# Performance work log

Measured on AMD Instinct MI355X. Metric: run time of the kernel, lower is better.

Reference implementation:

```python
import jax, jax.numpy as jnp
import numpy as np

N = 20000    # nodes
F = 64       # channels (num_features)
Z = 10       # species
DEG = 16
E = N * DEG  # edges
RD = 8       # radial_dim
EPS = 0.25   # epsilon (avg-degree normalization)
SQRT3 = 3.0 ** 0.5


def setup_inputs() -> dict:
    key = jax.random.key(0)
    ks = jax.random.split(key, 22)
    g = lambda i, shape, s=1.0: jax.random.normal(ks[i], shape, jnp.float32) * s
    return dict(
        vectors=g(0, (E, 3)),
        node_s=g(1, (N, F)),
        node_v=g(2, (N, F, 3)),
        radial_embed=jax.random.uniform(ks[3], (E, RD), jnp.float32),
        senders=jax.random.randint(ks[4], (E,), 0, N),
        receivers=jax.random.randint(ks[5], (E,), 0, N),
        species_counts=jnp.full((Z,), N // Z, dtype=jnp.int32),
        Wup0=g(6, (F, F)), Wup1=g(7, (F, F)),
        R1=g(8, (RD, 64)), R2=g(9, (64, 64)), R3=g(10, (64, 64)), R4=g(11, (64, 4 * F)),
        Wd0=g(12, (F, F)), Wd1=g(13, (F, F)),
        Ws0=g(14, (Z, F, F)), Ws1=g(15, (Z, F, F)),
        Wsc=g(16, (Z, 9, F)), Proj=g(17, (9, 9), 1.0 / 3.0),
        Wl0=g(18, (F, F)), Wl1=g(19, (F, F)),
        Wr=g(20, (F, 1)),
    )


def _forward(vectors, node_s, node_v, radial_embed, senders, receivers,
             species_counts, Wup0, Wup1, R1, R2, R3, R4, Wd0, Wd1,
             Ws0, Ws1, Wsc, Proj, Wl0, Wl1, Wr):
    inv = 1.0 / np.sqrt(F)
    # species index per node (counts -> contiguous blocks), like jnp.repeat in SymmetricContraction
    sidx = jnp.repeat(jnp.arange(Z), species_counts, total_repeat_length=N)

    # spherical harmonics l=0 (constant 1, folded into weights) and l=1
    r = jnp.linalg.norm(vectors, axis=-1, keepdims=True)
    Y1 = SQRT3 * vectors / r                              # (E,3)

    # species-indexed skip connection on input feats
    skip_s = jnp.einsum('nf,nfg->ng', node_s, Ws0[sidx]) * inv
    skip_v = jnp.einsum('nfi,nfg->ngi', node_v, Ws1[sidx]) * inv

    # linear_up (per-irrep channel mixing)
    hs = (node_s @ Wup0) * inv                            # (N,F)
    hv = jnp.einsum('nfi,fg->ngi', node_v, Wup1) * inv    # (N,F,3)

    # radial MLP -> per-edge, per-path, per-channel TP weights (weight_numel = 4*F)
    a = jax.nn.silu(radial_embed @ R1)
    a = jax.nn.silu(a @ R2)
    a = jax.nn.silu(a @ R3)
    w = (a @ R4).reshape(E, 4, F)

    # channelwise tensor product: gather senders, 4 CG paths, scatter to receivers
    es = hs[senders]                                      # (E,F)
    ev = hv[senders]                                      # (E,F,3)
    m_s = w[:, 0] * es + w[:, 1] * (jnp.einsum('efi,ei->ef', ev, Y1) / SQRT3)
    m_v = w[:, 2][..., None] * ev + w[:, 3][..., None] * (es[..., None] * Y1[:, None, :]) / SQRT3
    hs = jax.ops.segment_sum(m_s, receivers, num_segments=N) * EPS
    hv = jax.ops.segment_sum(m_v, receivers, num_segments=N) * EPS

    # linear_down
    hs = (hs @ Wd0) * inv
    hv = jnp.einsum('nfi,fg->ngi', hv, Wd1) * inv

    # symmetric contraction (correlation 1..3), species-keyed weights through fixed projection
    wsc = jnp.einsum('zpu,pb->zbu', Wsc, Proj)[sidx]      # (N,9,F)
    vv = jnp.sum(hv * hv, -1)                             # (N,F)
    bs = jnp.stack([hs, hs * hs, vv, hs ** 3, hs * vv], axis=1)                    # (N,5,F)
    bv = jnp.stack([hv, hs[..., None] * hv, (hs * hs)[..., None] * hv,
                    vv[..., None] * hv], axis=1)                                   # (N,4,F,3)
    cs = jnp.einsum('nbf,nbf->nf', bs, wsc[:, :5])
    cv = jnp.einsum('nbfi,nbf->nfi', bv, wsc[:, 5:])

    # linear_sc
    cs = (cs @ Wl0) * inv
    cv = jnp.einsum('nfi,fg->ngi', cv, Wl1) * inv

    # add skip
    h_s = cs + skip_s
    h_v = cv + skip_v

    # readout (0e -> 1x0e; only scalars participate)
    out = (h_s @ Wr) * inv                                # (N,1)
    return out, h_s, h_v


def reference(vectors, node_s, node_v, radial_embed, senders, receivers,
              species_counts, Wup0, Wup1, R1, R2, R3, R4, Wd0, Wd1,
              Ws0, Ws1, Wsc, Proj, Wl0, Wl1, Wr):
    return _forward(vectors, node_s, node_v, radial_embed, senders, receivers,
                    species_counts, Wup0, Wup1, R1, R2, R3, R4, Wd0, Wd1,
                    Ws0, Ws1, Wsc, Proj, Wl0, Wl1, Wr)
```

## Files before the change

### kernel.cpp

```cpp
#include <hip/hip_runtime.h>
#include <hip/hip_bf16.h>
#include <math.h>

#define N_NODES 20000
#define FCH 64
#define ZSP 10
#define E_EDGES 320000
#define CHUNK 160000
#define RDIM 8
#define EPSC 0.25f
#define SQRT3C 1.7320508075688772f
#define INV_SQRT3C 0.57735026918962576f
#define INV_F 0.125f

#define OFF_HSUP   0
#define OFF_HVUP   (N_NODES*64)
#define OFF_SKS    (OFF_HVUP + N_NODES*192)
#define OFF_SKV    (OFF_SKS + N_NODES*64)
#define OFF_HSMID  (OFF_SKV + N_NODES*192)
#define OFF_HVMID  (OFF_HSMID + N_NODES*64)
#define OFF_WSCP   (OFF_HVMID + N_NODES*192)
#define OFF_FRAGS  (OFF_WSCP + ZSP*576)
#define OFF_WBUF   (OFF_FRAGS + 13312)
#define OFF_CSR    (OFF_WBUF + CHUNK*128)
#define OFF_WF     (OFF_CSR + 2*CHUNK*4 + 400260)
#define CSR_CNT0   0
#define CSR_CNT1   20000
#define CSR_PTR0   40000
#define CSR_PTR1   60001
#define CSR_SEID   80002
#define CSR_AUX    400002

#define SU_WSC   5760
#define SU_PREP  (SU_WSC + 3328)
#define SU_PREP2 (SU_PREP + 26624)
#define SU_HIST  (SU_PREP2 + E_EDGES)

typedef __attribute__((ext_vector_type(8))) short bhalf8;
typedef __attribute__((ext_vector_type(4))) float f32x4;

__device__ __forceinline__ float silu_f(float x) {
    float e = __builtin_amdgcn_exp2f(x * -1.442695040888963f);
    return x * __builtin_amdgcn_rcpf(1.0f + e);
}

__device__ __forceinline__ unsigned short f2bf(float x) {
    unsigned int u = __float_as_uint(x);
    unsigned int r = u + 0x7FFFu + ((u >> 16) & 1u);
    return (unsigned short)(r >> 16);
}

__device__ __forceinline__ unsigned int pack_bf2(float lo, float hi) {
    __hip_bfloat162 b = __float22bfloat162_rn(make_float2(lo, hi));
    return *(unsigned int*)&b;
}

__device__ __forceinline__ void split_f32(float x, short& h, short& l) {
    unsigned int u = __float_as_uint(x);
    unsigned int hb = u & 0xFFFF0000u;
    h = (short)(u >> 16);
    float r = x - __uint_as_float(hb);
    l = (short)(__float_as_uint(r) >> 16);
}

__device__ __forceinline__ int species_of(int n, const int* counts) {
    int acc = 0, s = ZSP - 1;
#pragma unroll
    for (int z = 0; z < ZSP; z++) {
        int c = counts[z];
        if (n >= acc && n < acc + c) s = z;
        acc += c;
    }
    return s;
}

__global__ __launch_bounds__(256) void k_setup(
    const float* __restrict__ Wsc, const float* __restrict__ Proj, float* __restrict__ wscp,
    const float* __restrict__ R1, const float* __restrict__ R2,
    const float* __restrict__ R3, const float* __restrict__ R4,
    unsigned short* __restrict__ frags,
    const float* __restrict__ Wup0, const float* __restrict__ Wup1,
    const float* __restrict__ Ws0, const float* __restrict__ Ws1,
    const float* __restrict__ Wd0, const float* __restrict__ Wd1,
    const float* __restrict__ Wl0, const float* __restrict__ Wl1,
    unsigned short* __restrict__ wf,
    const int* __restrict__ receivers, int* __restrict__ csr) {
    int gid = blockIdx.x * 256 + threadIdx.x;
    if (gid < SU_WSC) {
        int z = gid / 576, t = gid % 576;
        int b = t >> 6, u = t & 63;
        float acc = 0.f;
#pragma unroll
        for (int p = 0; p < 9; p++) acc += Wsc[z * 576 + p * 64 + u] * Proj[p * 9 + b];
        wscp[z * 576 + b * 64 + u] = acc;
    } else if (gid < SU_PREP) {
        int id = gid - SU_WSC;
        int lane = id & 63, fi = id >> 6;
        int quad = lane >> 4, l15 = lane & 15;
        const float* W;
        int s, t, N;
        bool r1 = false;
        if (fi < 4)       { W = R1; s = 0; t = fi; N = 64; r1 = true; }
        else if (fi < 12) { W = R2; int x = fi - 4;  s = x >> 2; t = x & 3;  N = 64; }
        else if (fi < 20) { W = R3; int x = fi - 12; s = x >> 2; t = x & 3;  N = 64; }
        else              { W = R4; int x = fi - 20; s = x >> 4; t = x & 15; N = 256; }
        unsigned int v[4];
#pragma unroll
        for (int jj = 0; jj < 4; jj++) {
            unsigned short pk2[2];
#pragma unroll
            for (int o = 0; o < 2; o++) {
                int j = jj * 2 + o;
                int k = s * 32 + quad * 8 + j, n = t * 16 + l15;
                float val = (r1 && k >= RDIM) ? 0.f : W[k * N + n];
                pk2[o] = f2bf(val);
            }
            v[jj] = (unsigned int)pk2[0] | ((unsigned int)pk2[1] << 16);
        }
        uint4 pk; pk.x = v[0]; pk.y = v[1]; pk.z = v[2]; pk.w = v[3];
        ((uint4*)frags)[id] = pk;
    } else if (gid < SU_PREP2) {
        int id = gid - SU_PREP;
        int lane = id & 63, slot = id >> 6;
        int t = slot & 3, s = (slot >> 2) & 1, part = (slot >> 3) & 1, mat = slot >> 4;
        int quad = lane >> 4, l15 = lane & 15;
        const float* W;
        if (mat == 0)       W = Wup0;
        else if (mat == 1)  W = Wup1;
        else if (mat < 12)  W = Ws0 + (mat - 2) * 4096;
        else if (mat < 22)  W = Ws1 + (mat - 12) * 4096;
        else if (mat == 22) W = Wd0;
        else if (mat == 23) W = Wd1;
        else if (mat == 24) W = Wl0;
        else                W = Wl1;
        unsigned int v[4];
#pragma unroll
        for (int jj = 0; jj < 4; jj++) {
            unsigned short pk2[2];
#pragma unroll
            for (int o = 0; o < 2; o++) {
                int j = jj * 2 + o;
                int k = s * 32 + quad * 8 + j, n = t * 16 + l15;
                float x = W[k * 64 + n];
                short h, l;
                split_f32(x, h, l);
                pk2[o] = part == 0 ? (unsigned short)h : (unsigned short)l;
            }
            v[jj] = (unsigned int)pk2[0] | ((unsigned int)pk2[1] << 16);
        }
        uint4 pk; pk.x = v[0]; pk.y = v[1]; pk.z = v[2]; pk.w = v[3];
        ((uint4*)wf)[id] = pk;
    } else if (gid < SU_HIST) {
        int e = gid - SU_PREP2;
        int base = (e < CHUNK) ? CSR_CNT0 : CSR_CNT1;
        atomicAdd(&csr[base + receivers[e]], 1);
    }
}

__global__ __launch_bounds__(256) void k_scan1(int* __restrict__ csr) {
    __shared__ int sb[256];
    int z = blockIdx.y, b = blockIdx.x, t = threadIdx.x;
    int i = b * 256 + t;
    int cb = z ? CSR_CNT1 : CSR_CNT0;
    int pb = z ? CSR_PTR1 : CSR_PTR0;
    int x = (i < N_NODES) ? csr[cb + i] : 0;
    sb[t] = x;
    __syncthreads();
#pragma unroll
    for (int off = 1; off < 256; off <<= 1) {
        int v = (t >= off) ? sb[t - off] : 0;
        __syncthreads();
        sb[t] += v;
        __syncthreads();
    }
    if (i < N_NODES) csr[pb + i] = sb[t] - x;
    if (t == 255) csr[CSR_AUX + z * 128 + b] = sb[255];
}

__global__ __launch_bounds__(128) void k_scan2(int* __restrict__ csr) {
    __shared__ int sb[128];
    int z = blockIdx.x, t = threadIdx.x;
    int pb = z ? CSR_PTR1 : CSR_PTR0;
    int x = (t < 79) ? csr[CSR_AUX + z * 128 + t] : 0;
    sb[t] = x;
    __syncthreads();
#pragma unroll
    for (int off = 1; off < 128; off <<= 1) {
        int v = (t >= off) ? sb[t - off] : 0;
        __syncthreads();
        sb[t] += v;
        __syncthreads();
    }
    csr[CSR_AUX + z * 128 + t] = sb[t] - x;
    if (t == 127) csr[pb + N_NODES] = sb[127];
}

__global__ __launch_bounds__(256) void k_scan3(int* __restrict__ csr) {
    int z = blockIdx.y, b = blockIdx.x, t = threadIdx.x;
    int i = b * 256 + t;
    if (i >= N_NODES) return;
    int cb = z ? CSR_CNT1 : CSR_CNT0;
    int pb = z ? CSR_PTR1 : CSR_PTR0;
    int v = csr[pb + i] + csr[CSR_AUX + z * 128 + b];
    csr[pb + i] = v;
    csr[cb + i] = v;
}

__global__ __launch_bounds__(256) void k_bucket(
    const float* __restrict__ vectors, const int* __restrict__ senders,
    const int* __restrict__ receivers, int* __restrict__ csr,
    float4* __restrict__ erec) {
    int e = blockIdx.x * 256 + threadIdx.x;
    if (e >= E_EDGES) return;
    int z = (e < CHUNK) ? 0 : 1;
    int base = z ? CSR_CNT1 : CSR_CNT0;
    int pos = atomicAdd(&csr[base + receivers[e]], 1);
    float v0 = vectors[e * 3 + 0], v1 = vectors[e * 3 + 1], v2 = vectors[e * 3 + 2];
    float s = SQRT3C * rsqrtf(v0 * v0 + v1 * v1 + v2 * v2);
    int idx = z * CHUNK + pos;
    csr[CSR_SEID + idx] = e;
    float4 r;
    r.x = v0 * s; r.y = v1 * s; r.z = v2 * s; r.w = __int_as_float(senders[e]);
    erec[idx] = r;
}

__global__ __launch_bounds__(256) void k_node_pre(
    const float* __restrict__ ns, const float* __restrict__ nv,
    const int* __restrict__ counts, const unsigned short* __restrict__ wf,
    float* __restrict__ ws) {
    int tid = threadIdx.x, w = tid >> 6, lane = tid & 63;
    int q = lane >> 4, l15 = lane & 15;
    int nw = blockIdx.x * 16;
    int sid = species_of(nw, counts);
    const f32x4 z4 = {0.f, 0.f, 0.f, 0.f};

    bhalf8 Ah[2], Al[2];
    if (w == 0) {
#pragma unroll
        for (int s = 0; s < 2; s++) {
            const float* rp = ns + (size_t)(nw + l15) * 64 + s * 32 + q * 8;
            float4 a = *(const float4*)rp, b = *(const float4*)(rp + 4);
            float x[8] = {a.x, a.y, a.z, a.w, b.x, b.y, b.z, b.w};
#pragma unroll
            for (int j = 0; j < 8; j++) { short h, l; split_f32(x[j], h, l); Ah[s][j] = h; Al[s][j] = l; }
        }
    } else {
        int i = w - 1;
#pragma unroll
        for (int s = 0; s < 2; s++) {
            const float* rp = nv + (size_t)(nw + l15) * 192 + i;
#pragma unroll
            for (int j = 0; j < 8; j++) {
                float x = rp[(s * 32 + q * 8 + j) * 3];
                short h, l; split_f32(x, h, l); Ah[s][j] = h; Al[s][j] = l;
            }
        }
    }

    const bhalf8* wfv = (const bhalf8*)wf;
    float* hs_up = ws + OFF_HSUP;
    float* hv_up = ws + OFF_HVUP;
    float* sks   = ws + OFF_SKS;
    float* skv   = ws + OFF_SKV;

#pragma unroll
    for (int m = 0; m < 2; m++) {
        int mat = (w == 0) ? (m == 0 ? 0 : 2 + sid) : (m == 0 ? 1 : 12 + sid);
        float* dst; int stride, off;
        if (w == 0) { dst = m == 0 ? hs_up : sks; stride = 64; off = 0; }
        else        { dst = m == 0 ? hv_up : skv; stride = 192; off = (w - 1) * 64; }
#pragma unroll
        for (int t = 0; t < 4; t++) {
            f32x4 acc = z4;
#pragma unroll
            for (int s = 0; s < 2; s++) {
                bhalf8 bh = wfv[(size_t)(mat * 16 + 0 + s * 4 + t) * 64 + lane];
                bhalf8 bl = wfv[(size_t)(mat * 16 + 8 + s * 4 + t) * 64 + lane];
                acc = __builtin_amdgcn_mfma_f32_16x16x32_bf16(Ah[s], bh, acc, 0, 0, 0);
                acc = __builtin_amdgcn_mfma_f32_16x16x32_bf16(Al[s], bh, acc, 0, 0, 0);
                acc = __builtin_amdgcn_mfma_f32_16x16x32_bf16(Ah[s], bl, acc, 0, 0, 0);
            }
#pragma unroll
            for (int r = 0; r < 4; r++)
                dst[(size_t)(nw + q * 4 + r) * stride + off + t * 16 + l15] = acc[r] * INV_F;
        }
    }
}

__global__ __launch_bounds__(256) void k_mlp(
    const float* __restrict__ radial, const unsigned short* __restrict__ frags,
    const int* __restrict__ csr, unsigned short* __restrict__ wbuf, int e_base) {
    __shared__ unsigned short r4lds[16384];
    __shared__ unsigned short act[4][16 * 72];
    int tid = threadIdx.x;
    int lane = tid & 63, w = tid >> 6, quad = lane >> 4, l15 = lane & 15;

    const uint4* r4g = (const uint4*)(frags + 20 * 64 * 8);
    uint4* r4l = (uint4*)r4lds;
    for (int i = tid; i < 2048; i += 256) r4l[i] = r4g[i];
    const bhalf8* fr = (const bhalf8*)frags;
    bhalf8 r1f[4], r2f[2][4], r3f[2][4];
#pragma unroll
    for (int t = 0; t < 4; t++) r1f[t] = fr[t * 64 + lane];
#pragma unroll
    for (int s = 0; s < 2; s++)
#pragma unroll
        for (int t = 0; t < 4; t++) {
            r2f[s][t] = fr[(4 + s * 4 + t) * 64 + lane];
            r3f[s][t] = fr[(12 + s * 4 + t) * 64 + lane];
        }
    __syncthreads();

    const f32x4 z4 = {0.f, 0.f, 0.f, 0.f};
    const bhalf8* r4f = (const bhalf8*)r4lds;
    unsigned short* actw = act[w];

    for (int it = 0; it < 2; it++) {
        int el0 = (blockIdx.x * 2 + it) * 64 + w * 16;
        bhalf8 af = {0, 0, 0, 0, 0, 0, 0, 0};
        if (quad == 0) {
            int eid = csr[CSR_SEID + e_base + el0 + l15];
            const float* rp = radial + (size_t)eid * 8;
            float4 ra = *(const float4*)rp;
            float4 rb = *(const float4*)(rp + 4);
            af[0] = (short)f2bf(ra.x); af[1] = (short)f2bf(ra.y);
            af[2] = (short)f2bf(ra.z); af[3] = (short)f2bf(ra.w);
            af[4] = (short)f2bf(rb.x); af[5] = (short)f2bf(rb.y);
            af[6] = (short)f2bf(rb.z); af[7] = (short)f2bf(rb.w);
        }
        {
            f32x4 acc[4];
#pragma unroll
            for (int t = 0; t < 4; t++)
                acc[t] = __builtin_amdgcn_mfma_f32_16x16x32_bf16(af, r1f[t], z4, 0, 0, 0);
#pragma unroll
            for (int t = 0; t < 4; t++)
#pragma unroll
                for (int r = 0; r < 4; r++)
                    actw[(quad * 4 + r) * 72 + t * 16 + l15] = f2bf(silu_f(acc[t][r]));
        }
#pragma unroll
        for (int layer = 0; layer < 2; layer++) {
            bhalf8 a0 = *(const bhalf8*)&actw[l15 * 72 + 0 + quad * 8];
            bhalf8 a1 = *(const bhalf8*)&actw[l15 * 72 + 32 + quad * 8];
            f32x4 acc[4];
#pragma unroll
            for (int t = 0; t < 4; t++) {
                bhalf8 b0 = layer == 0 ? r2f[0][t] : r3f[0][t];
                bhalf8 b1 = layer == 0 ? r2f[1][t] : r3f[1][t];
                acc[t] = __builtin_amdgcn_mfma_f32_16x16x32_bf16(
                    a1, b1, __builtin_amdgcn_mfma_f32_16x16x32_bf16(a0, b0, z4, 0, 0, 0), 0, 0, 0);
            }
#pragma unroll
            for (int t = 0; t < 4; t++)
#pragma unroll
                for (int r = 0; r < 4; r++)
                    actw[(quad * 4 + r) * 72 + t * 16 + l15] = f2bf(silu_f(acc[t][r]));
        }
        {
            bhalf8 a0 = *(const bhalf8*)&actw[l15 * 72 + 0 + quad * 8];
            bhalf8 a1 = *(const bhalf8*)&actw[l15 * 72 + 32 + quad * 8];
            unsigned int d0[16];
#pragma unroll
            for (int h = 0; h < 2; h++) {
                f32x4 acc8[8];
#pragma unroll
                for (int t8 = 0; t8 < 8; t8++) {
                    int t = h * 8 + t8;
                    acc8[t8] = __builtin_amdgcn_mfma_f32_16x16x32_bf16(
                        a1, r4f[(16 + t) * 64 + lane],
                        __builtin_amdgcn_mfma_f32_16x16x32_bf16(a0, r4f[t * 64 + lane], z4, 0, 0, 0),
                        0, 0, 0);
                }
#pragma unroll
                for (int t4 = 0; t4 < 4; t4++)
#pragma unroll
                    for (int r = 0; r < 4; r++) {
                        unsigned int d = pack_bf2(acc8[t4][r], acc8[t4 + 4][r]);
                        if (h == 0) {
                            d0[t4 * 4 + r] = d;
                        } else {
                            int el = el0 + quad * 4 + r;
                            int f = t4 * 16 + l15;
                            uint2 pk; pk.x = d0[t4 * 4 + r]; pk.y = d;
                            ((uint2*)wbuf)[(size_t)el * 64 + f] = pk;
                        }
                    }
            }
        }
    }
}

__global__ __launch_bounds__(256) void k_tp_gather(
    const unsigned short* __restrict__ wbuf, const int* __restrict__ csr,
    const float4* __restrict__ erec, float* __restrict__ ws,
    int z, int accum) {
    int tid = threadIdx.x, w = tid >> 6, f = tid & 63;
    int n = blockIdx.x * 4 + w;
    const float* hs_up = ws + OFF_HSUP;
    const float* hv_up = ws + OFF_HVUP;
    float* hs_mid = ws + OFF_HSMID;
    float* hv_mid = ws + OFF_HVMID;
    int pb = z ? CSR_PTR1 : CSR_PTR0;
    int beg = csr[pb + n], end = csr[pb + n + 1];
    int e_base = z * CHUNK;
    float ams = 0.f, am0 = 0.f, am1 = 0.f, am2 = 0.f;

    if (beg < end) {
        int last = end - 1;
        float4 rcA = erec[e_base + beg];
        uint2 wrA = ((const uint2*)wbuf)[(size_t)beg * 64 + f];
        int sxA = __float_as_int(rcA.w);
        float esA = hs_up[sxA * 64 + f];
        float eA0 = hv_up[sxA * 192 + f];
        float eA1 = hv_up[sxA * 192 + 64 + f];
        float eA2 = hv_up[sxA * 192 + 128 + f];
        int j1 = (beg + 1 < end) ? beg + 1 : last;
        float4 rcB = erec[e_base + j1];
        uint2 wrB = ((const uint2*)wbuf)[(size_t)j1 * 64 + f];
        int sxB = __float_as_int(rcB.w);
        float esB = hs_up[sxB * 64 + f];
        float eB0 = hv_up[sxB * 192 + f];
        float eB1 = hv_up[sxB * 192 + 64 + f];
        float eB2 = hv_up[sxB * 192 + 128 + f];

        for (int i = beg; i < end; i++) {
            int j2 = (i + 2 < end) ? i + 2 : last;
            float4 rcC = erec[e_base + j2];
            uint2 wrC = ((const uint2*)wbuf)[(size_t)j2 * 64 + f];
            int sxC = __float_as_int(rcC.w);
            float esC = hs_up[sxC * 64 + f];
            float eC0 = hv_up[sxC * 192 + f];
            float eC1 = hv_up[sxC * 192 + 64 + f];
            float eC2 = hv_up[sxC * 192 + 128 + f];
            float w0 = __uint_as_float(wrA.x << 16);
            float w1 = __uint_as_float(wrA.x & 0xFFFF0000u);
            float w2 = __uint_as_float(wrA.y << 16);
            float w3 = __uint_as_float(wrA.y & 0xFFFF0000u);
            float dot = eA0 * rcA.x + eA1 * rcA.y + eA2 * rcA.z;
            ams += w0 * esA + w1 * dot * INV_SQRT3C;
            float t3 = w3 * esA * INV_SQRT3C;
            am0 += w2 * eA0 + t3 * rcA.x;
            am1 += w2 * eA1 + t3 * rcA.y;
            am2 += w2 * eA2 + t3 * rcA.z;
            rcA = rcB; wrA = wrB; esA = esB; eA0 = eB0; eA1 = eB1; eA2 = eB2;
            rcB = rcC; wrB = wrC; esB = esC; eB0 = eC0; eB1 = eC1; eB2 = eC2;
        }
    }
    if (!accum) {
        hs_mid[n * 64 + f] = ams;
        hv_mid[n * 192 + f] = am0;
        hv_mid[n * 192 + 64 + f] = am1;
        hv_mid[n * 192 + 128 + f] = am2;
    } else {
        hs_mid[n * 64 + f] = (hs_mid[n * 64 + f] + ams) * EPSC;
        hv_mid[n * 192 + f] = (hv_mid[n * 192 + f] + am0) * EPSC;
        hv_mid[n * 192 + 64 + f] = (hv_mid[n * 192 + 64 + f] + am1) * EPSC;
        hv_mid[n * 192 + 128 + f] = (hv_mid[n * 192 + 128 + f] + am2) * EPSC;
    }
}

__global__ __launch_bounds__(256) void k_node_post(
    const int* __restrict__ counts, const unsigned short* __restrict__ wf,
    const float* __restrict__ Wr, float* __restrict__ ws, float* __restrict__ out) {
    __shared__ float T[4][16][68];
    int tid = threadIdx.x, w = tid >> 6, lane = tid & 63;
    int q = lane >> 4, l15 = lane & 15;
    int nw = blockIdx.x * 16;
    int sid = species_of(nw, counts);
    const f32x4 z4 = {0.f, 0.f, 0.f, 0.f};
    const bhalf8* wfv = (const bhalf8*)wf;
    const float* hs_mid = ws + OFF_HSMID;
    const float* hv_mid = ws + OFF_HVMID;
    const float* sks = ws + OFF_SKS;
    const float* skv = ws + OFF_SKV;
    const float* wscp = ws + OFF_WSCP;

    {
        const float* src = (w == 0) ? hs_mid + (size_t)nw * 64
                                    : hv_mid + (size_t)nw * 192 + (w - 1) * 64;
        int rstride = (w == 0) ? 64 : 192;
        bhalf8 Ah[2], Al[2];
#pragma unroll
        for (int s = 0; s < 2; s++) {
            const float* rp = src + (size_t)l15 * rstride + s * 32 + q * 8;
            float4 a = *(const float4*)rp, b = *(const float4*)(rp + 4);
            float x[8] = {a.x, a.y, a.z, a.w, b.x, b.y, b.z, b.w};
#pragma unroll
            for (int j = 0; j < 8; j++) { short h, l; split_f32(x[j], h, l); Ah[s][j] = h; Al[s][j] = l; }
        }
        int mat = (w == 0) ? 22 : 23;
#pragma unroll
        for (int t = 0; t < 4; t++) {
            f32x4 acc = z4;
#pragma unroll
            for (int s = 0; s < 2; s++) {
                bhalf8 bh = wfv[(size_t)(mat * 16 + 0 + s * 4 + t) * 64 + lane];
                bhalf8 bl = wfv[(size_t)(mat * 16 + 8 + s * 4 + t) * 64 + lane];
                acc = __builtin_amdgcn_mfma_f32_16x16x32_bf16(Ah[s], bh, acc, 0, 0, 0);
                acc = __builtin_amdgcn_mfma_f32_16x16x32_bf16(Al[s], bh, acc, 0, 0, 0);
                acc = __builtin_amdgcn_mfma_f32_16x16x32_bf16(Ah[s], bl, acc, 0, 0, 0);
            }
#pragma unroll
            for (int r = 0; r < 4; r++)
                T[w][q * 4 + r][t * 16 + l15] = acc[r] * INV_F;
        }
    }
    __syncthreads();

    {
        int col = tid & 63, rg = tid >> 6;
        float wv[9];
#pragma unroll
        for (int b = 0; b < 9; b++) wv[b] = wscp[sid * 576 + b * 64 + col];
#pragma unroll
        for (int rr = 0; rr < 4; rr++) {
            int row = rg * 4 + rr;
            float hs = T[0][row][col];
            float h0 = T[1][row][col], h1 = T[2][row][col], h2 = T[3][row][col];
            float vv = h0 * h0 + h1 * h1 + h2 * h2;
            float cs = wv[0] * hs + wv[1] * hs * hs + wv[2] * vv
                     + wv[3] * hs * hs * hs + wv[4] * hs * vv;
            float fv = wv[5] + wv[6] * hs + wv[7] * hs * hs + wv[8] * vv;
            T[0][row][col] = cs;
            T[1][row][col] = h0 * fv;
            T[2][row][col] = h1 * fv;
            T[3][row][col] = h2 * fv;
        }
    }
    __syncthreads();

    {
        bhalf8 Ah[2], Al[2];
#pragma unroll
        for (int s = 0; s < 2; s++) {
            const float* rp = &T[w][l15][s * 32 + q * 8];
            float4 a = *(const float4*)rp, b = *(const float4*)(rp + 4);
            float x[8] = {a.x, a.y, a.z, a.w, b.x, b.y, b.z, b.w};
#pragma unroll
            for (int j = 0; j < 8; j++) { short h, l; split_f32(x[j], h, l); Ah[s][j] = h; Al[s][j] = l; }
        }
        int mat = (w == 0) ? 24 : 25;
        float* d_hs = out + N_NODES;
        float* d_hv = out + N_NODES + N_NODES * 64;
        float p[4] = {0.f, 0.f, 0.f, 0.f};
#pragma unroll
        for (int t = 0; t < 4; t++) {
            f32x4 acc = z4;
#pragma unroll
            for (int s = 0; s < 2; s++) {
                bhalf8 bh = wfv[(size_t)(mat * 16 + 0 + s * 4 + t) * 64 + lane];
                bhalf8 bl = wfv[(size_t)(mat * 16 + 8 + s * 4 + t) * 64 + lane];
                acc = __builtin_amdgcn_mfma_f32_16x16x32_bf16(Ah[s], bh, acc, 0, 0, 0);
                acc = __builtin_amdgcn_mfma_f32_16x16x32_bf16(Al[s], bh, acc, 0, 0, 0);
                acc = __builtin_amdgcn_mfma_f32_16x16x32_bf16(Ah[s], bl, acc, 0, 0, 0);
            }
            int col = t * 16 + l15;
            if (w == 0) {
                float wr = Wr[col];
#pragma unroll
                for (int r = 0; r < 4; r++) {
                    int gn = nw + q * 4 + r;
                    float v = acc[r] * INV_F + sks[(size_t)gn * 64 + col];
                    d_hs[(size_t)gn * 64 + col] = v;
                    p[r] += v * wr;
                }
            } else {
                int i = w - 1;
#pragma unroll
                for (int r = 0; r < 4; r++) {
                    int gn = nw + q * 4 + r;
                    float v = acc[r] * INV_F + skv[(size_t)gn * 192 + i * 64 + col];
                    d_hv[(size_t)gn * 192 + col * 3 + i] = v;
                }
            }
        }
        if (w == 0) {
#pragma unroll
            for (int r = 0; r < 4; r++) {
#pragma unroll
                for (int off = 1; off < 16; off <<= 1) p[r] += __shfl_xor(p[r], off, 64);
                if (l15 == 0) out[nw + q * 4 + r] = p[r] * INV_F;
            }
        }
    }
}

extern "C" void kernel_launch(void* const* d_in, const int* in_sizes, int n_in,
                              void* d_out, int out_size, void* d_ws, size_t ws_size,
                              hipStream_t stream) {
    const float* vectors   = (const float*)d_in[0];
    const float* node_s    = (const float*)d_in[1];
    const float* node_v    = (const float*)d_in[2];
    const float* radial    = (const float*)d_in[3];
    const int*   senders   = (const int*)d_in[4];
    const int*   receivers = (const int*)d_in[5];
    const int*   counts    = (const int*)d_in[6];
    const float* Wup0 = (const float*)d_in[7];
    const float* Wup1 = (const float*)d_in[8];
    const float* R1   = (const float*)d_in[9];
    const float* R2   = (const float*)d_in[10];
    const float* R3   = (const float*)d_in[11];
    const float* R4   = (const float*)d_in[12];
    const float* Wd0  = (const float*)d_in[13];
    const float* Wd1  = (const float*)d_in[14];
    const float* Ws0  = (const float*)d_in[15];
    const float* Ws1  = (const float*)d_in[16];
    const float* Wsc  = (const float*)d_in[17];
    const float* Proj = (const float*)d_in[18];
    const float* Wl0  = (const float*)d_in[19];
    const float* Wl1  = (const float*)d_in[20];
    const float* Wr   = (const float*)d_in[21];
    float* ws  = (float*)d_ws;
    float* out = (float*)d_out;
    unsigned short* frags = (unsigned short*)(ws + OFF_FRAGS);
    unsigned short* wbuf  = (unsigned short*)(ws + OFF_WBUF);
    float4* erec = (float4*)(ws + OFF_CSR);
    int* csr = (int*)(ws + OFF_CSR + 2 * CHUNK * 4);
    unsigned short* wf = (unsigned short*)(ws + OFF_WF);

    hipMemsetAsync(csr, 0, 2 * N_NODES * sizeof(int), stream);
    k_setup<<<(SU_HIST + 255) / 256, 256, 0, stream>>>(
        Wsc, Proj, ws + OFF_WSCP, R1, R2, R3, R4, frags,
        Wup0, Wup1, Ws0, Ws1, Wd0, Wd1, Wl0, Wl1, wf, receivers, csr);
    k_scan1<<<dim3(79, 2), 256, 0, stream>>>(csr);
    k_scan2<<<2, 128, 0, stream>>>(csr);
    k_scan3<<<dim3(79, 2), 256, 0, stream>>>(csr);
    k_bucket<<<E_EDGES / 256, 256, 0, stream>>>(vectors, senders, receivers, csr, erec);
    k_node_pre<<<N_NODES / 16, 256, 0, stream>>>(node_s, node_v, counts, wf, ws);
    for (int c = 0; c < 2; c++) {
        k_mlp<<<1250, 256, 0, stream>>>(radial, frags, csr, wbuf, c * CHUNK);
        k_tp_gather<<<N_NODES / 4, 256, 0, stream>>>(wbuf, csr, erec, ws, c, c);
    }
    k_node_post<<<N_NODES / 16, 256, 0, stream>>>(counts, wf, Wr, ws, out);
}
```

Before: 340.1 us.

## Keep radial MLP activations in registers via transposed MFMA and lane shuffles

The radial MLP kernel swaps MFMA operand order so each layer's output is produced transposed. Activations are packed to bf16 in registers and redistributed to the next layer's fragment layout with cross-lane shuffles, removing the per-wave LDS activation buffer and its store/load round trips. Each block now handles one 64-edge tile instead of looping over two, so the grid size is doubled. The cost is more shuffle instructions and selects, plus twice as many blocks that each reload the R4 weights into LDS.

```diff
diff --git a/kernel.cpp b/kernel.cpp
--- a/kernel.cpp
+++ b/kernel.cpp
@@ -55,6 +55,11 @@
     return *(unsigned int*)&b;
 }
 
+__device__ __forceinline__ bhalf8 mk8(unsigned a, unsigned b, unsigned c, unsigned d) {
+    uint4 u; u.x = a; u.y = b; u.z = c; u.w = d;
+    return *(bhalf8*)&u;
+}
+
 __device__ __forceinline__ void split_f32(float x, short& h, short& l) {
     unsigned int u = __float_as_uint(x);
     unsigned int hb = u & 0xFFFF0000u;
@@ -287,11 +292,27 @@
     }
 }
 
+template<int S>
+__device__ __forceinline__ bhalf8 xfrag(const unsigned* pkA, const unsigned* pkB,
+                                        int q, int l15) {
+    int L0 = ((q & 1) << 5) + l15;
+    int L1 = L0 + 16;
+    bool hi = (q >> 1) != 0;
+    unsigned a0 = (unsigned)__shfl((int)pkA[2 * S], L0, 64);
+    unsigned a1 = (unsigned)__shfl((int)pkA[2 * S + 1], L0, 64);
+    unsigned b0 = (unsigned)__shfl((int)pkB[2 * S], L0, 64);
+    unsigned b1 = (unsigned)__shfl((int)pkB[2 * S + 1], L0, 64);
+    unsigned c0 = (unsigned)__shfl((int)pkA[2 * S], L1, 64);
+    unsigned c1 = (unsigned)__shfl((int)pkA[2 * S + 1], L1, 64);
+    unsigned e0 = (unsigned)__shfl((int)pkB[2 * S], L1, 64);
+    unsigned e1 = (unsigned)__shfl((int)pkB[2 * S + 1], L1, 64);
+    return mk8(hi ? a1 : a0, hi ? b1 : b0, hi ? c1 : c0, hi ? e1 : e0);
+}
+
 __global__ __launch_bounds__(256) void k_mlp(
     const float* __restrict__ radial, const unsigned short* __restrict__ frags,
     const int* __restrict__ csr, unsigned short* __restrict__ wbuf, int e_base) {
     __shared__ unsigned short r4lds[16384];
-    __shared__ unsigned short act[4][16 * 72];
     int tid = threadIdx.x;
     int lane = tid & 63, w = tid >> 6, quad = lane >> 4, l15 = lane & 15;
 
@@ -313,79 +334,75 @@
 
     const f32x4 z4 = {0.f, 0.f, 0.f, 0.f};
     const bhalf8* r4f = (const bhalf8*)r4lds;
-    unsigned short* actw = act[w];
-
-    for (int it = 0; it < 2; it++) {
-        int el0 = (blockIdx.x * 2 + it) * 64 + w * 16;
-        bhalf8 af = {0, 0, 0, 0, 0, 0, 0, 0};
-        if (quad == 0) {
-            int eid = csr[CSR_SEID + e_base + el0 + l15];
-            const float* rp = radial + (size_t)eid * 8;
-            float4 ra = *(const float4*)rp;
-            float4 rb = *(const float4*)(rp + 4);
-            af[0] = (short)f2bf(ra.x); af[1] = (short)f2bf(ra.y);
-            af[2] = (short)f2bf(ra.z); af[3] = (short)f2bf(ra.w);
-            af[4] = (short)f2bf(rb.x); af[5] = (short)f2bf(rb.y);
-            af[6] = (short)f2bf(rb.z); af[7] = (short)f2bf(rb.w);
-        }
-        {
-            f32x4 acc[4];
-#pragma unroll
-            for (int t = 0; t < 4; t++)
-                acc[t] = __builtin_amdgcn_mfma_f32_16x16x32_bf16(af, r1f[t], z4, 0, 0, 0);
-#pragma unroll
-            for (int t = 0; t < 4; t++)
-#pragma unroll
-                for (int r = 0; r < 4; r++)
-                    actw[(quad * 4 + r) * 72 + t * 16 + l15] = f2bf(silu_f(acc[t][r]));
-        }
-#pragma unroll
-        for (int layer = 0; layer < 2; layer++) {
-            bhalf8 a0 = *(const bhalf8*)&actw[l15 * 72 + 0 + quad * 8];
-            bhalf8 a1 = *(const bhalf8*)&actw[l15 * 72 + 32 + quad * 8];
-            f32x4 acc[4];
-#pragma unroll
-            for (int t = 0; t < 4; t++) {
-                bhalf8 b0 = layer == 0 ? r2f[0][t] : r3f[0][t];
-                bhalf8 b1 = layer == 0 ? r2f[1][t] : r3f[1][t];
-                acc[t] = __builtin_amdgcn_mfma_f32_16x16x32_bf16(
-                    a1, b1, __builtin_amdgcn_mfma_f32_16x16x32_bf16(a0, b0, z4, 0, 0, 0), 0, 0, 0);
-            }
-#pragma unroll
-            for (int t = 0; t < 4; t++)
-#pragma unroll
-                for (int r = 0; r < 4; r++)
-                    actw[(quad * 4 + r) * 72 + t * 16 + l15] = f2bf(silu_f(acc[t][r]));
-        }
-        {
-            bhalf8 a0 = *(const bhalf8*)&actw[l15 * 72 + 0 + quad * 8];
-            bhalf8 a1 = *(const bhalf8*)&actw[l15 * 72 + 32 + quad * 8];
-            unsigned int d0[16];
-#pragma unroll
-            for (int h = 0; h < 2; h++) {
-                f32x4 acc8[8];
-#pragma unroll
-                for (int t8 = 0; t8 < 8; t8++) {
-                    int t = h * 8 + t8;
-                    acc8[t8] = __builtin_amdgcn_mfma_f32_16x16x32_bf16(
-                        a1, r4f[(16 + t) * 64 + lane],
-                        __builtin_amdgcn_mfma_f32_16x16x32_bf16(a0, r4f[t * 64 + lane], z4, 0, 0, 0),
-                        0, 0, 0);
-                }
-#pragma unroll
-                for (int t4 = 0; t4 < 4; t4++)
-#pragma unroll
-                    for (int r = 0; r < 4; r++) {
-                        unsigned int d = pack_bf2(acc8[t4][r], acc8[t4 + 4][r]);
-                        if (h == 0) {
-                            d0[t4 * 4 + r] = d;
-                        } else {
-                            int el = el0 + quad * 4 + r;
-                            int f = t4 * 16 + l15;
-                            uint2 pk; pk.x = d0[t4 * 4 + r]; pk.y = d;
-                            ((uint2*)wbuf)[(size_t)el * 64 + f] = pk;
-                        }
-                    }
+
+    int el0 = (blockIdx.x * 4 + w) * 16;
+
+    bhalf8 af = {0, 0, 0, 0, 0, 0, 0, 0};
+    if (quad == 0) {
+        int eid = csr[CSR_SEID + e_base + el0 + l15];
+        const float* rp = radial + (size_t)eid * 8;
+        float4 ra = *(const float4*)rp;
+        float4 rb = *(const float4*)(rp + 4);
+        af[0] = (short)f2bf(ra.x); af[1] = (short)f2bf(ra.y);
+        af[2] = (short)f2bf(ra.z); af[3] = (short)f2bf(ra.w);
+        af[4] = (short)f2bf(rb.x); af[5] = (short)f2bf(rb.y);
+        af[6] = (short)f2bf(rb.z); af[7] = (short)f2bf(rb.w);
+    }
+    unsigned pkA[4], pkB[4];
+    {
+        f32x4 acc[4];
+#pragma unroll
+        for (int t = 0; t < 4; t++)
+            acc[t] = __builtin_amdgcn_mfma_f32_16x16x32_bf16(r1f[t], af, z4, 0, 0, 0);
+#pragma unroll
+        for (int t = 0; t < 4; t++) {
+            pkA[t] = pack_bf2(silu_f(acc[t][0]), silu_f(acc[t][1]));
+            pkB[t] = pack_bf2(silu_f(acc[t][2]), silu_f(acc[t][3]));
+        }
+    }
+#pragma unroll
+    for (int layer = 0; layer < 2; layer++) {
+        bhalf8 b0 = xfrag<0>(pkA, pkB, quad, l15);
+        bhalf8 b1 = xfrag<1>(pkA, pkB, quad, l15);
+        f32x4 acc[4];
+#pragma unroll
+        for (int t = 0; t < 4; t++) {
+            bhalf8 w0 = layer == 0 ? r2f[0][t] : r3f[0][t];
+            bhalf8 w1 = layer == 0 ? r2f[1][t] : r3f[1][t];
+            acc[t] = __builtin_amdgcn_mfma_f32_16x16x32_bf16(
+                w1, b1, __builtin_amdgcn_mfma_f32_16x16x32_bf16(w0, b0, z4, 0, 0, 0), 0, 0, 0);
+        }
+#pragma unroll
+        for (int t = 0; t < 4; t++) {
+            pkA[t] = pack_bf2(silu_f(acc[t][0]), silu_f(acc[t][1]));
+            pkB[t] = pack_bf2(silu_f(acc[t][2]), silu_f(acc[t][3]));
+        }
+    }
+    {
+        bhalf8 a0 = xfrag<0>(pkA, pkB, quad, l15);
+        bhalf8 a1 = xfrag<1>(pkA, pkB, quad, l15);
+#pragma unroll
+        for (int t4 = 0; t4 < 4; t4++) {
+            f32x4 p0 = __builtin_amdgcn_mfma_f32_16x16x32_bf16(
+                a1, r4f[(16 + t4) * 64 + lane],
+                __builtin_amdgcn_mfma_f32_16x16x32_bf16(a0, r4f[t4 * 64 + lane], z4, 0, 0, 0), 0, 0, 0);
+            f32x4 p1 = __builtin_amdgcn_mfma_f32_16x16x32_bf16(
+                a1, r4f[(20 + t4) * 64 + lane],
+                __builtin_amdgcn_mfma_f32_16x16x32_bf16(a0, r4f[(4 + t4) * 64 + lane], z4, 0, 0, 0), 0, 0, 0);
+            f32x4 p2 = __builtin_amdgcn_mfma_f32_16x16x32_bf16(
+                a1, r4f[(24 + t4) * 64 + lane],
+                __builtin_amdgcn_mfma_f32_16x16x32_bf16(a0, r4f[(8 + t4) * 64 + lane], z4, 0, 0, 0), 0, 0, 0);
+            f32x4 p3 = __builtin_amdgcn_mfma_f32_16x16x32_bf16(
+                a1, r4f[(28 + t4) * 64 + lane],
+                __builtin_amdgcn_mfma_f32_16x16x32_bf16(a0, r4f[(12 + t4) * 64 + lane], z4, 0, 0, 0), 0, 0, 0);
+#pragma unroll
+            for (int r = 0; r < 4; r++) {
+                int el = el0 + quad * 4 + r;
+                int f = t4 * 16 + l15;
+                uint2 pk;
+                pk.x = pack_bf2(p0[r], p1[r]);
+                pk.y = pack_bf2(p2[r], p3[r]);
+                ((uint2*)wbuf)[(size_t)el * 64 + f] = pk;
             }
         }
     }
@@ -629,7 +646,7 @@
     k_bucket<<<E_EDGES / 256, 256, 0, stream>>>(vectors, senders, receivers, csr, erec);
     k_node_pre<<<N_NODES / 16, 256, 0, stream>>>(node_s, node_v, counts, wf, ws);
     for (int c = 0; c < 2; c++) {
-        k_mlp<<<1250, 256, 0, stream>>>(radial, frags, csr, wbuf, c * CHUNK);
+        k_mlp<<<2500, 256, 0, stream>>>(radial, frags, csr, wbuf, c * CHUNK);
         k_tp_gather<<<N_NODES / 4, 256, 0, stream>>>(wbuf, csr, erec, ws, c, c);
     }
     k_node_post<<<N_NODES / 16, 256, 0, stream>>>(counts, wf, Wr, ws, out);
```

New measurement: 333.5 us. Within noise of the previous version (-1.9%).
